# Optimization experiments

Hardware: AMD Instinct MI355X
Metric: run time of the kernel (lower is better)

Reference implementation:

```python
import math
import jax, jax.numpy as jnp
import numpy as np

B, DIM, C, N = 1024, 512, 1000, 8
R = 0.05
WEIGHT_LAMBDA = 0.3
CN = C * N
TOPK = math.ceil(R * CN)  # 400


def setup_inputs() -> dict:
    key = jax.random.key(0)
    k1, k2, k3 = jax.random.split(key, 3)
    x = jax.random.normal(k1, (B, DIM), dtype=jnp.float32)
    # kaiming_uniform_(a=sqrt(5)) on a (DIM, CN) tensor: fan_in = CN (torch 2D fan_in = size(1)),
    # gain = sqrt(2/(1+a^2)) = sqrt(1/3), bound = gain * sqrt(3/fan_in)
    bound = math.sqrt(1.0 / 3.0) * math.sqrt(3.0 / CN)
    proxies = jax.random.uniform(k2, (DIM, CN), dtype=jnp.float32, minval=-bound, maxval=bound)
    target = jax.random.randint(k3, (B,), 0, C)
    return {"x": x, "proxies": proxies, "target": target}


def reference(x, proxies, target):
    instance_label = jnp.repeat(jnp.arange(C), N)  # (CN,)

    # F.normalize(Proxies, p=2, dim=0) with eps=1e-12 clamp
    norm = jnp.maximum(jnp.linalg.norm(proxies, axis=0, keepdims=True), 1e-12)
    centers = proxies / norm  # (DIM, CN)

    similarity = x @ centers  # (B, CN)

    positive_mask = (target[:, None] == instance_label[None, :]).astype(similarity.dtype)

    # topk over similarity boosted so all positives are included, then scatter 1s
    _, idx = jax.lax.top_k(similarity + 1000.0 * positive_mask, TOPK)  # (B, TOPK)
    mask = jnp.zeros_like(similarity).at[jnp.arange(B)[:, None], idx].set(1.0)
    mask = jax.lax.stop_gradient(mask)

    prob_a = mask * similarity  # (B, CN)
    # matmul with block one-hot y_instance_onehot == sum over the N proxies of each class
    logits = prob_a.reshape(B, C, N).sum(axis=-1)  # (B, C)

    logits_mask = jax.lax.stop_gradient((logits != 0.0).astype(logits.dtype))
    exp_l = jnp.exp(logits) * logits_mask
    predict = exp_l / (1e-8 + exp_l.sum(axis=1, keepdims=True))

    # sum(-y_onehot * log(predict+1e-20), 1) == -log(predict[b, target[b]] + 1e-20)
    loss_classify = jnp.mean(-jnp.log(predict[jnp.arange(B), target] + 1e-20))

    # regularizer: (centers.T @ centers) @ y_instance_onehot, fused as
    # centers.T @ (per-class sum of centers) -- identical math, avoids the CNxCN matrix
    centers_cls = centers.reshape(DIM, C, N).sum(axis=-1)  # (DIM, C)
    centers_logits = centers.T @ centers_cls  # (CN, C)
    logp = jax.nn.log_softmax(centers_logits, axis=1)
    reg = -jnp.mean(logp[jnp.arange(CN), instance_label])

    total = loss_classify + WEIGHT_LAMBDA * reg
    return (total, loss_classify)
```

## Files before the change

### kernel.cpp

```cpp
#include <hip/hip_runtime.h>
#include <hip/hip_bf16.h>
#include <math.h>

#define PB   1024
#define PDIM 512
#define PC   1000
#define PN   8
#define PCN  8000
#define PTOPK 400
#define NONPOS_K 392
#define NBIN 1024
#define CANDMAX 1024

typedef __bf16 bf16x8 __attribute__((ext_vector_type(8)));
typedef __bf16 bf16x4 __attribute__((ext_vector_type(4)));
typedef float  f32x4  __attribute__((ext_vector_type(4)));

__device__ static inline void async_load16(const __bf16* g, __bf16* l) {
    __builtin_amdgcn_global_load_lds(
        (const __attribute__((address_space(1))) void*)g,
        (__attribute__((address_space(3))) void*)l,
        16, 0, 0);
}

__global__ __launch_bounds__(256) void k_pre(const float* __restrict__ x,
                                             const float* __restrict__ P,
                                             __bf16* __restrict__ xb,
                                             float* __restrict__ ssqp,
                                             float* __restrict__ esd,
                                             float* __restrict__ padf,
                                             float* __restrict__ acc) {
    int b = blockIdx.x, tid = threadIdx.x;
    if (b == 0 && tid < 8) acc[tid] = 0.f;
    if (b < 512) {
        int i = b * 256 + tid;
        float4 v = ((const float4*)x)[i];
        bf16x4 o;
        o[0] = (__bf16)v.x; o[1] = (__bf16)v.y; o[2] = (__bf16)v.z; o[3] = (__bf16)v.w;
        ((bf16x4*)xb)[i] = o;
    } else if (b < 768) {
        int idx = b - 512;
        int slice = idx & 7, jb = idx >> 3;
        int j = jb * 256 + tid;
        if (j < PCN) {
            const float* p = P + (size_t)(slice * 64) * PCN + j;
            float ss = 0.f;
#pragma unroll 8
            for (int r = 0; r < 64; ++r) {
                float v = p[(size_t)r * PCN];
                ss = fmaf(v, v, ss);
            }
            ssqp[slice * PCN + j] = ss;
        }
    } else {
        int i = (b - 768) * 256 + tid;
        if (i < 16000) esd[i] = 0.f;
        else if (i < 16000 + 6144) padf[i - 16000] = 0.f;
    }
}

__global__ __launch_bounds__(256) void k_tpose(const float* __restrict__ P,
                                               const float* __restrict__ ssqp,
                                               __bf16* __restrict__ Pt,
                                               __bf16* __restrict__ ccls) {
    __shared__ float t[64][65];
    __shared__ float sinv[64];
    int tid = threadIdx.x;
    int tx = tid & 63, ty = tid >> 6;
    int j0 = blockIdx.x * 64, d0 = blockIdx.y * 64;
    if (tid < 64) {
        float sq = 0.f;
#pragma unroll
        for (int p2 = 0; p2 < 8; ++p2) sq += ssqp[p2 * PCN + j0 + tid];
        sinv[tid] = 1.0f / fmaxf(sqrtf(sq), 1e-12f);
    }
#pragma unroll
    for (int r = 0; r < 16; ++r) {
        int d = d0 + ty * 16 + r;
        t[ty * 16 + r][tx] = P[(size_t)d * PCN + j0 + tx];
    }
    __syncthreads();
    float cs0 = 0.f, cs1 = 0.f;
#pragma unroll
    for (int r = 0; r < 16; ++r) {
        int jl = ty * 16 + r;
        float val = t[tx][jl] * sinv[jl];
        Pt[(size_t)(j0 + jl) * PDIM + d0 + tx] = (__bf16)val;
        if (r < 8) cs0 += val; else cs1 += val;
    }
    int c0 = (j0 >> 3) + ty * 2;
    ccls[(size_t)c0 * PDIM + d0 + tx] = (__bf16)cs0;
    ccls[(size_t)(c0 + 1) * PDIM + d0 + tx] = (__bf16)cs1;
}

#define GEMM_STAGE(A, Bt, Ma, Nb, m0, n0, buf, k0) {                          \
    _Pragma("unroll")                                                         \
    for (int pass = 0; pass < 2; ++pass) {                                    \
        int cc_ = pass * 256 + w * 64 + lane;                                 \
        int arow = (m0) + (cc_ >> 2); if (arow > (Ma) - 1) arow = (Ma) - 1;   \
        async_load16((A) + (size_t)arow * PDIM + (k0) + (cc_ & 3) * 8,        \
                     &As[buf][cc_ * 8]);                                      \
        int brow = (n0) + (cc_ >> 2); if (brow > (Nb) - 1) brow = (Nb) - 1;   \
        async_load16((Bt) + (size_t)brow * PDIM + (k0) + (cc_ & 3) * 8,       \
                     &Bs[buf][cc_ * 8]);                                      \
    } }

#define GEMM_CORE(A, Bt, Ma, Nb, m0, n0)                                      \
    GEMM_STAGE(A, Bt, Ma, Nb, m0, n0, 0, 0)                                   \
    for (int it = 0; it < 16; ++it) {                                         \
        int cur = it & 1;                                                     \
        __syncthreads();                                                      \
        if (it < 15) GEMM_STAGE(A, Bt, Ma, Nb, m0, n0, cur ^ 1, (it + 1) * 32)\
        bf16x8 av[4], bv[4];                                                  \
        _Pragma("unroll")                                                     \
        for (int i = 0; i < 4; ++i) {                                         \
            av[i] = *(const bf16x8*)&As[cur][(wr * 64 + i * 16 + l15) * 32 + quad * 8]; \
            bv[i] = *(const bf16x8*)&Bs[cur][(wc * 64 + i * 16 + l15) * 32 + quad * 8]; \
        }                                                                     \
        _Pragma("unroll")                                                     \
        for (int i = 0; i < 4; ++i)                                           \
            _Pragma("unroll")                                                 \
            for (int j = 0; j < 4; ++j)                                       \
                acc[i][j] = __builtin_amdgcn_mfma_f32_16x16x32_bf16(          \
                    av[i], bv[j], acc[i][j], 0, 0, 0);                        \
    }

__global__ __launch_bounds__(256) void k_gemms(const __bf16* __restrict__ xb,
                                               const __bf16* __restrict__ Pt,
                                               const __bf16* __restrict__ ccls,
                                               __bf16* __restrict__ simb,
                                               float* __restrict__ esum,
                                               float* __restrict__ diag) {
    __shared__ __bf16 As[2][128 * 32];
    __shared__ __bf16 Bs[2][128 * 32];
    int tid = threadIdx.x;
    int w = tid >> 6, lane = tid & 63;
    int wr = w >> 1, wc = w & 1;
    int quad = lane >> 4, l15 = lane & 15;
    f32x4 acc[4][4] = {};
    int id = blockIdx.x;
    if (id < 504) {
        int n0 = (id % 8) * 128, m0 = (id / 8) * 128;
        GEMM_CORE(Pt, ccls, PCN, PB, m0, n0)
#pragma unroll
        for (int i = 0; i < 4; ++i) {
            int r0 = m0 + wr * 64 + i * 16 + quad * 4;
            float psum[4] = {0.f, 0.f, 0.f, 0.f};
#pragma unroll
            for (int j = 0; j < 4; ++j) {
                int cc = n0 + wc * 64 + j * 16 + l15;
                bool cvalid = (cc < PC);
#pragma unroll
                for (int r = 0; r < 4; ++r) {
                    float v = acc[i][j][r];
                    psum[r] += cvalid ? expf(v) : 0.f;
                    int rr = r0 + r;
                    if (cvalid && rr < PCN && cc == (rr >> 3)) diag[rr] = v;
                }
            }
#pragma unroll
            for (int off = 1; off < 16; off <<= 1)
#pragma unroll
                for (int r = 0; r < 4; ++r)
                    psum[r] += __shfl_xor(psum[r], off, 64);
            if (l15 == 0) {
#pragma unroll
                for (int r = 0; r < 4; ++r) {
                    int rr = r0 + r;
                    if (rr < PCN) atomicAdd(&esum[rr], psum[r]);
                }
            }
        }
    } else {
        int id2 = id - 504;
        int n0 = (id2 % 63) * 128, m0 = (id2 / 63) * 128;
        GEMM_CORE(xb, Pt, PB, PCN, m0, n0)
#pragma unroll
        for (int i = 0; i < 4; ++i) {
            int r0 = m0 + wr * 64 + i * 16 + quad * 4;
#pragma unroll
            for (int j = 0; j < 4; ++j) {
                int cc = n0 + wc * 64 + j * 16 + l15;
                if (cc < PCN) {
#pragma unroll
                    for (int r = 0; r < 4; ++r)
                        simb[(size_t)(r0 + r) * PCN + cc] = (__bf16)acc[i][j][r];
                }
            }
        }
    }
}

__global__ __launch_bounds__(256) void k_rowloss(const __bf16* __restrict__ sim,
                                                 const int* __restrict__ target,
                                                 float* __restrict__ acc) {
    __shared__ unsigned hist[NBIN];
    __shared__ float redf[8];
    __shared__ unsigned wtot[4];
    __shared__ float cand[CANDMAX];
    __shared__ unsigned candn;
    __shared__ int s_bin, s_A;
    __shared__ float s_tau;
    __shared__ int s_gt, s_eq;
    __shared__ float s_et;

    int b = blockIdx.x, tid = threadIdx.x;
    int lane = tid & 63, wv = tid >> 6;
    const bf16x8* row8 = (const bf16x8*)(sim + (size_t)b * PCN);
    int targ = target[b];

#pragma unroll
    for (int k = 0; k < 4; ++k) hist[tid + 256 * k] = 0u;
    if (tid == 0) candn = 0u;

    float pv[4][8];
    float lmn = INFINITY, lmx = -INFINITY;
#pragma unroll
    for (int k = 0; k < 4; ++k) {
        int c = tid + 256 * k;
        if (c < PC) {
            bf16x8 vv = row8[c];
#pragma unroll
            for (int n = 0; n < 8; ++n) pv[k][n] = (float)vv[n];
            if (c != targ) {
#pragma unroll
                for (int n = 0; n < 8; ++n) {
                    lmn = fminf(lmn, pv[k][n]);
                    lmx = fmaxf(lmx, pv[k][n]);
                }
            }
        } else {
#pragma unroll
            for (int n = 0; n < 8; ++n) pv[k][n] = 0.f;
        }
    }
    for (int off = 32; off; off >>= 1) {
        lmn = fminf(lmn, __shfl_down(lmn, off, 64));
        lmx = fmaxf(lmx, __shfl_down(lmx, off, 64));
    }
    if (lane == 0) { redf[wv] = lmn; redf[4 + wv] = lmx; }
    __syncthreads();
    float lo = fminf(fminf(redf[0], redf[1]), fminf(redf[2], redf[3]));
    float hi = fmaxf(fmaxf(redf[4], redf[5]), fmaxf(redf[6], redf[7]));
    float range = hi - lo;
    float scale = (range > 0.f) ? (float)NBIN / range : 0.f;

#pragma unroll
    for (int k = 0; k < 4; ++k) {
        int c = tid + 256 * k;
        if (c < PC && c != targ) {
#pragma unroll
            for (int n = 0; n < 8; ++n) {
                int bin = (int)((pv[k][n] - lo) * scale);
                bin = bin < 0 ? 0 : (bin > NBIN - 1 ? NBIN - 1 : bin);
                atomicAdd(&hist[bin], 1u);
            }
        }
    }
    __syncthreads();

    int b0 = tid * 4;
    unsigned h0 = hist[b0], h1 = hist[b0 + 1], h2 = hist[b0 + 2], h3 = hist[b0 + 3];
    unsigned l3 = h3, l2 = h2 + l3, l1 = h1 + l2, l0 = h0 + l1;
    unsigned T = l0;
#pragma unroll
    for (int step = 1; step < 64; step <<= 1) {
        unsigned u = __shfl_down(T, step, 64);
        if (lane + step < 64) T += u;
    }
    if (lane == 0) wtot[wv] = T;
    __syncthreads();
    unsigned tail = 0;
#pragma unroll
    for (int w2 = 0; w2 < 4; ++w2) if (w2 > wv) tail += wtot[w2];
    unsigned E = T - l0 + tail;
    {
        unsigned sfx[4] = {l0 + E, l1 + E, l2 + E, l3 + E};
        unsigned nxt[4] = {l1 + E, l2 + E, l3 + E, E};
#pragma unroll
        for (int i = 0; i < 4; ++i)
            if (sfx[i] >= NONPOS_K && nxt[i] < NONPOS_K) {
                s_bin = b0 + i;
                s_A = (int)nxt[i];
            }
    }
    __syncthreads();
    int tbin = s_bin, A = s_A;

#pragma unroll
    for (int k = 0; k < 4; ++k) {
        int c = tid + 256 * k;
        if (c < PC && c != targ) {
#pragma unroll
            for (int n = 0; n < 8; ++n) {
                int bin = (int)((pv[k][n] - lo) * scale);
                bin = bin < 0 ? 0 : (bin > NBIN - 1 ? NBIN - 1 : bin);
                if (bin == tbin) {
                    unsigned idx = atomicAdd(&candn, 1u);
                    if (idx < CANDMAX) cand[idx] = pv[k][n];
                }
            }
        }
    }
    __syncthreads();
    int m = (int)candn; if (m > CANDMAX) m = CANDMAX;
    int rank = NONPOS_K - A;
    for (int ci = tid; ci < m; ci += 256) {
        float val = cand[ci];
        int g = 0, e = 0;
        for (int i = 0; i < m; ++i) {
            g += cand[i] > val;
            e += cand[i] == val;
        }
        if (g < rank && rank <= g + e) { s_tau = val; s_gt = g; s_eq = e; }
    }
    __syncthreads();
    float tau = s_tau;
    int cgt = A + s_gt, ceq = s_eq;
    int rem = NONPOS_K - cgt;
    bool all_eq = (rem >= ceq);

    int offs[4] = {0, 0, 0, 0};
    if (!all_eq) {
        unsigned chunk_base = 0;
#pragma unroll
        for (int k = 0; k < 4; ++k) {
            int c = tid + 256 * k;
            unsigned tn = 0;
            if (c < PC && c != targ) {
#pragma unroll
                for (int n = 0; n < 8; ++n) tn += (pv[k][n] == tau) ? 1u : 0u;
            }
            unsigned inc = tn;
#pragma unroll
            for (int step = 1; step < 64; step <<= 1) {
                unsigned u = __shfl_up(inc, step, 64);
                if (lane >= step) inc += u;
            }
            __syncthreads();
            if (lane == 63) wtot[wv] = inc;
            __syncthreads();
            unsigned base = 0;
#pragma unroll
            for (int w2 = 0; w2 < 4; ++w2) if (w2 < wv) base += wtot[w2];
            offs[k] = (int)(chunk_base + base + inc - tn);
            chunk_base += wtot[0] + wtot[1] + wtot[2] + wtot[3];
        }
    }

    float psum = 0.f;
#pragma unroll
    for (int k = 0; k < 4; ++k) {
        int c = tid + 256 * k;
        if (c >= PC) continue;
        float lg = 0.f;
        if (c == targ) {
#pragma unroll
            for (int n = 0; n < 8; ++n) lg += pv[k][n];
        } else {
#pragma unroll
            for (int n = 0; n < 8; ++n) {
                float v = pv[k][n];
                bool sel = v > tau;
                if (!sel && v == tau) {
                    if (all_eq) sel = true;
                    else { sel = (offs[k] < rem); offs[k]++; }
                }
                if (sel) lg += v;
            }
        }
        float e = (lg != 0.0f) ? expf(lg) : 0.0f;
        psum += e;
        if (c == targ) s_et = e;
    }
    for (int off = 32; off; off >>= 1) psum += __shfl_down(psum, off, 64);
    if (lane == 0) redf[wv] = psum;
    __syncthreads();
    if (tid == 0) {
        float denom = 1e-8f + redf[0] + redf[1] + redf[2] + redf[3];
        atomicAdd(acc, -logf(s_et / denom + 1e-20f));
    }
}

__global__ __launch_bounds__(256) void k_final(const float* __restrict__ esum,
                                               const float* __restrict__ diag,
                                               const float* __restrict__ acc,
                                               float* __restrict__ out) {
    __shared__ float redf[4];
    int tid = threadIdx.x, lane = tid & 63, wv = tid >> 6;
    float s = 0.f;
    for (int j = tid; j < PCN; j += 256)
        s += logf(esum[j]) - diag[j];
    for (int off = 32; off; off >>= 1) s += __shfl_down(s, off, 64);
    if (lane == 0) redf[wv] = s;
    __syncthreads();
    if (tid == 0) {
        float rg = (redf[0] + redf[1] + redf[2] + redf[3]) * (1.0f / PCN);
        float lc = acc[0] * (1.0f / PB);
        out[0] = lc + 0.3f * rg;
        out[1] = lc;
    }
}

extern "C" void kernel_launch(void* const* d_in, const int* in_sizes, int n_in,
                              void* d_out, int out_size, void* d_ws, size_t ws_size,
                              hipStream_t stream) {
    const float* x       = (const float*)d_in[0];
    const float* proxies = (const float*)d_in[1];
    const int*   target  = (const int*)d_in[2];
    float* out = (float*)d_out;
    float* ws  = (float*)d_ws;

    float*  acc   = ws;
    float*  ssqp  = ws + 64;
    float*  esum  = ws + 64064;
    float*  diag  = ws + 72064;
    __bf16* xb    = (__bf16*)(ws + 80064);
    __bf16* cclsb = (__bf16*)(ws + 342208);
    __bf16* Pt    = (__bf16*)(ws + 604352);
    __bf16* simb  = (__bf16*)(ws + 2652352);

    float* padf = (float*)cclsb + 256000;

    k_pre<<<856, 256, 0, stream>>>(x, proxies, xb, ssqp, esum, padf, acc);
    k_tpose<<<dim3(125, 8), 256, 0, stream>>>(proxies, ssqp, Pt, cclsb);

    k_gemms<<<1008, 256, 0, stream>>>(xb, Pt, cclsb, simb, esum, diag);

    k_rowloss<<<PB, 256, 0, stream>>>(simb, target, acc);
    k_final<<<1, 256, 0, stream>>>(esum, diag, acc, out);
}
```

Measured before the change: 145.3 us.

## Fuse both GEMMs into one block sharing the loaded proxy tile

The two GEMMs (x·centers and centers^T·class-centers) were handled by separate blocks, and each loaded the proxy tile on its own. Now each block computes both products for the same 128-row proxy tile and reads that tile from LDS as both the B operand and the A operand. The grid is halved to 504 blocks, and each block holds two accumulator sets and three LDS buffers, so register pressure is higher and the launch bound is set to 2 blocks per CU. The intent is to cut global-to-LDS traffic for the proxy matrix. In exchange there are fewer, heavier blocks and the risk of register spills.

```diff
diff --git a/kernel.cpp b/kernel.cpp
--- a/kernel.cpp
+++ b/kernel.cpp
@@ -93,99 +93,105 @@
     ccls[(size_t)(c0 + 1) * PDIM + d0 + tx] = (__bf16)cs1;
 }
 
-#define GEMM_STAGE(A, Bt, Ma, Nb, m0, n0, buf, k0) {                          \
-    _Pragma("unroll")                                                         \
-    for (int pass = 0; pass < 2; ++pass) {                                    \
-        int cc_ = pass * 256 + w * 64 + lane;                                 \
-        int arow = (m0) + (cc_ >> 2); if (arow > (Ma) - 1) arow = (Ma) - 1;   \
-        async_load16((A) + (size_t)arow * PDIM + (k0) + (cc_ & 3) * 8,        \
-                     &As[buf][cc_ * 8]);                                      \
-        int brow = (n0) + (cc_ >> 2); if (brow > (Nb) - 1) brow = (Nb) - 1;   \
-        async_load16((Bt) + (size_t)brow * PDIM + (k0) + (cc_ & 3) * 8,       \
-                     &Bs[buf][cc_ * 8]);                                      \
-    } }
-
-#define GEMM_CORE(A, Bt, Ma, Nb, m0, n0)                                      \
-    GEMM_STAGE(A, Bt, Ma, Nb, m0, n0, 0, 0)                                   \
-    for (int it = 0; it < 16; ++it) {                                         \
-        int cur = it & 1;                                                     \
-        __syncthreads();                                                      \
-        if (it < 15) GEMM_STAGE(A, Bt, Ma, Nb, m0, n0, cur ^ 1, (it + 1) * 32)\
-        bf16x8 av[4], bv[4];                                                  \
-        _Pragma("unroll")                                                     \
-        for (int i = 0; i < 4; ++i) {                                         \
-            av[i] = *(const bf16x8*)&As[cur][(wr * 64 + i * 16 + l15) * 32 + quad * 8]; \
-            bv[i] = *(const bf16x8*)&Bs[cur][(wc * 64 + i * 16 + l15) * 32 + quad * 8]; \
-        }                                                                     \
-        _Pragma("unroll")                                                     \
-        for (int i = 0; i < 4; ++i)                                           \
-            _Pragma("unroll")                                                 \
-            for (int j = 0; j < 4; ++j)                                       \
-                acc[i][j] = __builtin_amdgcn_mfma_f32_16x16x32_bf16(          \
-                    av[i], bv[j], acc[i][j], 0, 0, 0);                        \
-    }
-
-__global__ __launch_bounds__(256) void k_gemms(const __bf16* __restrict__ xb,
-                                               const __bf16* __restrict__ Pt,
-                                               const __bf16* __restrict__ ccls,
-                                               __bf16* __restrict__ simb,
-                                               float* __restrict__ esum,
-                                               float* __restrict__ diag) {
-    __shared__ __bf16 As[2][128 * 32];
-    __shared__ __bf16 Bs[2][128 * 32];
+__global__ __launch_bounds__(256, 2) void k_gemms(const __bf16* __restrict__ xb,
+                                                  const __bf16* __restrict__ Pt,
+                                                  const __bf16* __restrict__ ccls,
+                                                  __bf16* __restrict__ simb,
+                                                  float* __restrict__ esum,
+                                                  float* __restrict__ diag) {
+    __shared__ __bf16 Xs[2][128 * 32];
+    __shared__ __bf16 Ps[2][128 * 32];
+    __shared__ __bf16 Cs[2][128 * 32];
     int tid = threadIdx.x;
     int w = tid >> 6, lane = tid & 63;
     int wr = w >> 1, wc = w & 1;
     int quad = lane >> 4, l15 = lane & 15;
-    f32x4 acc[4][4] = {};
     int id = blockIdx.x;
-    if (id < 504) {
-        int n0 = (id % 8) * 128, m0 = (id / 8) * 128;
-        GEMM_CORE(Pt, ccls, PCN, PB, m0, n0)
+    int jt = id >> 3, t = id & 7;
+    int m0 = t * 128;
+    int n0 = jt * 128;
+
+    f32x4 accS[4][4] = {};
+    f32x4 accC[4][4] = {};
+
+#define STAGE3(buf, k0) {                                                     \
+    _Pragma("unroll")                                                         \
+    for (int pass = 0; pass < 2; ++pass) {                                    \
+        int cc_ = pass * 256 + w * 64 + lane;                                 \
+        int row_ = cc_ >> 2, ko_ = (cc_ & 3) * 8;                             \
+        async_load16(xb + (size_t)(m0 + row_) * PDIM + (k0) + ko_,            \
+                     &Xs[buf][cc_ * 8]);                                      \
+        int prow = n0 + row_; if (prow > PCN - 1) prow = PCN - 1;             \
+        async_load16(Pt + (size_t)prow * PDIM + (k0) + ko_,                   \
+                     &Ps[buf][cc_ * 8]);                                      \
+        async_load16(ccls + (size_t)(m0 + row_) * PDIM + (k0) + ko_,          \
+                     &Cs[buf][cc_ * 8]);                                      \
+    } }
+
+    STAGE3(0, 0)
+    for (int it = 0; it < 16; ++it) {
+        int cur = it & 1;
+        __syncthreads();
+        if (it < 15) STAGE3(cur ^ 1, (it + 1) * 32)
+        bf16x8 xa[4], pb[4], pa[4], cb[4];
 #pragma unroll
         for (int i = 0; i < 4; ++i) {
-            int r0 = m0 + wr * 64 + i * 16 + quad * 4;
-            float psum[4] = {0.f, 0.f, 0.f, 0.f};
+            xa[i] = *(const bf16x8*)&Xs[cur][(wr * 64 + i * 16 + l15) * 32 + quad * 8];
+            pb[i] = *(const bf16x8*)&Ps[cur][(wc * 64 + i * 16 + l15) * 32 + quad * 8];
+            pa[i] = *(const bf16x8*)&Ps[cur][(wr * 64 + i * 16 + l15) * 32 + quad * 8];
+            cb[i] = *(const bf16x8*)&Cs[cur][(wc * 64 + i * 16 + l15) * 32 + quad * 8];
+        }
+#pragma unroll
+        for (int i = 0; i < 4; ++i)
 #pragma unroll
             for (int j = 0; j < 4; ++j) {
-                int cc = n0 + wc * 64 + j * 16 + l15;
-                bool cvalid = (cc < PC);
-#pragma unroll
-                for (int r = 0; r < 4; ++r) {
-                    float v = acc[i][j][r];
-                    psum[r] += cvalid ? expf(v) : 0.f;
-                    int rr = r0 + r;
-                    if (cvalid && rr < PCN && cc == (rr >> 3)) diag[rr] = v;
-                }
-            }
-#pragma unroll
-            for (int off = 1; off < 16; off <<= 1)
+                accS[i][j] = __builtin_amdgcn_mfma_f32_16x16x32_bf16(
+                    xa[i], pb[j], accS[i][j], 0, 0, 0);
+                accC[i][j] = __builtin_amdgcn_mfma_f32_16x16x32_bf16(
+                    pa[i], cb[j], accC[i][j], 0, 0, 0);
+            }
+    }
+#undef STAGE3
+
+#pragma unroll
+    for (int i = 0; i < 4; ++i) {
+        int r0 = m0 + wr * 64 + i * 16 + quad * 4;
+#pragma unroll
+        for (int j = 0; j < 4; ++j) {
+            int cc = n0 + wc * 64 + j * 16 + l15;
+            if (cc < PCN) {
 #pragma unroll
                 for (int r = 0; r < 4; ++r)
-                    psum[r] += __shfl_xor(psum[r], off, 64);
-            if (l15 == 0) {
-#pragma unroll
-                for (int r = 0; r < 4; ++r) {
-                    int rr = r0 + r;
-                    if (rr < PCN) atomicAdd(&esum[rr], psum[r]);
-                }
-            }
-        }
-    } else {
-        int id2 = id - 504;
-        int n0 = (id2 % 63) * 128, m0 = (id2 / 63) * 128;
-        GEMM_CORE(xb, Pt, PB, PCN, m0, n0)
-#pragma unroll
-        for (int i = 0; i < 4; ++i) {
-            int r0 = m0 + wr * 64 + i * 16 + quad * 4;
-#pragma unroll
-            for (int j = 0; j < 4; ++j) {
-                int cc = n0 + wc * 64 + j * 16 + l15;
-                if (cc < PCN) {
-#pragma unroll
-                    for (int r = 0; r < 4; ++r)
-                        simb[(size_t)(r0 + r) * PCN + cc] = (__bf16)acc[i][j][r];
-                }
+                    simb[(size_t)(r0 + r) * PCN + cc] = (__bf16)accS[i][j][r];
+            }
+        }
+    }
+#pragma unroll
+    for (int i = 0; i < 4; ++i) {
+        int r0 = n0 + wr * 64 + i * 16 + quad * 4;
+        float psum[4] = {0.f, 0.f, 0.f, 0.f};
+#pragma unroll
+        for (int j = 0; j < 4; ++j) {
+            int cc = m0 + wc * 64 + j * 16 + l15;
+            bool cvalid = (cc < PC);
+#pragma unroll
+            for (int r = 0; r < 4; ++r) {
+                float v = accC[i][j][r];
+                psum[r] += cvalid ? expf(v) : 0.f;
+                int rr = r0 + r;
+                if (cvalid && rr < PCN && cc == (rr >> 3)) diag[rr] = v;
+            }
+        }
+#pragma unroll
+        for (int off = 1; off < 16; off <<= 1)
+#pragma unroll
+            for (int r = 0; r < 4; ++r)
+                psum[r] += __shfl_xor(psum[r], off, 64);
+        if (l15 == 0) {
+#pragma unroll
+            for (int r = 0; r < 4; ++r) {
+                int rr = r0 + r;
+                if (rr < PCN) atomicAdd(&esum[rr], psum[r]);
             }
         }
     }
@@ -425,7 +431,7 @@
     k_pre<<<856, 256, 0, stream>>>(x, proxies, xb, ssqp, esum, padf, acc);
     k_tpose<<<dim3(125, 8), 256, 0, stream>>>(proxies, ssqp, Pt, cclsb);
 
-    k_gemms<<<1008, 256, 0, stream>>>(xb, Pt, cclsb, simb, esum, diag);
+    k_gemms<<<504, 256, 0, stream>>>(xb, Pt, cclsb, simb, esum, diag);
 
     k_rowloss<<<PB, 256, 0, stream>>>(simb, target, acc);
     k_final<<<1, 256, 0, stream>>>(esum, diag, acc, out);
```

Result: faster. 140.2 us, median of 2 (-3.5%).
